# Kernel tuning notes

Measured on AMD Instinct MI355X. Metric: run time of the kernel, lower is better.

The kernel has to match this reference:

```python
import jax, jax.numpy as jnp
import numpy as np

N = 50000      # nodes
E = 800000     # edges (avg degree 16)
D_IN = 64
D_H = 64


def setup_inputs() -> dict:
    key = jax.random.key(0)
    k = jax.random.split(key, 4)
    x = jax.random.normal(k[0], (N, D_IN), dtype=jnp.float32)
    edge_index = jax.random.randint(k[1], (2, E), 0, N, dtype=jnp.int64)
    W1 = jax.random.normal(k[2], (D_IN, D_H), dtype=jnp.float32) * (1.0 / np.sqrt(D_IN))
    b1 = jnp.zeros((D_H,), dtype=jnp.float32)
    W2 = jax.random.normal(k[3], (D_H, 1), dtype=jnp.float32) * (1.0 / np.sqrt(D_H))
    b2 = jnp.zeros((1,), dtype=jnp.float32)
    return {"x": x, "edge_index": edge_index, "W1": W1, "b1": b1, "W2": W2, "b2": b2}


def gcn_conv(x, src, dst, W, b):
    """PyG-style GCNConv: linear -> symmetric-normalized scatter-aggregate + bias.
    src/dst already include self-loops."""
    n = x.shape[0]
    h = x @ W                                                   # [N, Dout]
    deg = jax.ops.segment_sum(jnp.ones_like(dst, dtype=h.dtype), dst, num_segments=n)
    dinv_sqrt = jnp.where(deg > 0, jax.lax.rsqrt(jnp.maximum(deg, 1e-12)), 0.0)
    norm = dinv_sqrt[src] * dinv_sqrt[dst]                       # [E+N]
    agg = jax.ops.segment_sum(h[src] * norm[:, None], dst, num_segments=n)
    return agg + b


def reference(x, edge_index, W1, b1, W2, b2):
    n = x.shape[0]
    loops = jnp.arange(n, dtype=edge_index.dtype)
    src = jnp.concatenate([edge_index[0], loops])                # add self-loops
    dst = jnp.concatenate([edge_index[1], loops])
    h = jax.nn.relu(gcn_conv(x, src, dst, W1, b1))               # [N, D_H]
    out = gcn_conv(h, src, dst, W2, b2)                          # [N, 1]
    return out.squeeze(-1)                                       # [N]
```

## Files before the change

kernel.cpp:

```cpp
#include <hip/hip_runtime.h>
#include <hip/hip_fp16.h>

#define D 64
#define PW2 256
#define PSH2 8
#define EPB 4096

__global__ void k_cast(const float4* __restrict__ x4, __half2* __restrict__ xh2,
                       int total4) {
    int i = blockIdx.x * blockDim.x + threadIdx.x;
    if (i < total4) {
        float4 v = x4[i];
        xh2[2 * i]     = __floats2half2_rn(v.x, v.y);
        xh2[2 * i + 1] = __floats2half2_rn(v.z, v.w);
    }
}

__global__ __launch_bounds__(256) void k_hist(const int* __restrict__ dst, int E,
                                              int* __restrict__ counts, int NP) {
    extern __shared__ int lh[];
    int t = threadIdx.x, b = blockIdx.x;
    for (int i = t; i < NP; i += 256) lh[i] = 0;
    __syncthreads();
    int base = b * EPB;
#pragma unroll
    for (int k = 0; k < EPB / 256; ++k) {
        int e = base + k * 256 + t;
        if (e < E) atomicAdd(&lh[dst[e] >> PSH2], 1);
    }
    __syncthreads();
    for (int i = t; i < NP; i += 256) counts[(size_t)b * NP + i] = lh[i];
}

__global__ __launch_bounds__(256) void k_scanA(int* __restrict__ counts, int NB, int NP,
                                               int* __restrict__ bin_total) {
    __shared__ int sh[256];
    int t = threadIdx.x, bin = blockIdx.x;
    int v = (t < NB) ? counts[(size_t)t * NP + bin] : 0;
    sh[t] = v;
    __syncthreads();
    for (int off = 1; off < 256; off <<= 1) {
        int u = (t >= off) ? sh[t - off] : 0;
        __syncthreads();
        sh[t] += u;
        __syncthreads();
    }
    if (t < NB) counts[(size_t)t * NP + bin] = sh[t] - v;
    if (t == 255) bin_total[bin] = sh[255];
}

__global__ __launch_bounds__(256) void k_scatter(const int* __restrict__ src,
        const int* __restrict__ dst, int E, const int* __restrict__ counts,
        const int* __restrict__ bin_total, int NP, int* __restrict__ csr_e) {
    __shared__ int bs[256];
    extern __shared__ int cur[];
    int t = threadIdx.x, b = blockIdx.x;
    int v = (t < NP) ? bin_total[t] : 0;
    bs[t] = v;
    __syncthreads();
    for (int off = 1; off < 256; off <<= 1) {
        int u = (t >= off) ? bs[t - off] : 0;
        __syncthreads();
        bs[t] += u;
        __syncthreads();
    }
    if (t < NP) cur[t] = counts[(size_t)b * NP + t] + (bs[t] - v);
    __syncthreads();
    int base = b * EPB;
#pragma unroll
    for (int k = 0; k < EPB / 256; ++k) {
        int e = base + k * 256 + t;
        if (e < E) {
            int s = src[e], d = dst[e];
            int pos = atomicAdd(&cur[d >> PSH2], 1);
            csr_e[pos] = s | ((d & (PW2 - 1)) << 16);
        }
    }
}

__global__ __launch_bounds__(256) void k_sort2(const int* __restrict__ csr_e,
        const int* __restrict__ bin_total, int NP, int n,
        int* __restrict__ csr_src, int* __restrict__ row_ptr,
        float* __restrict__ dinv) {
    __shared__ int bs[256];
    __shared__ int cnt[PW2];
    __shared__ int sh[PW2];
    __shared__ int cursor[PW2];
    __shared__ int s_beg, s_end;
    int t = threadIdx.x, p = blockIdx.x;
    int bv = (t < NP) ? bin_total[t] : 0;
    bs[t] = bv;
    __syncthreads();
    for (int off = 1; off < 256; off <<= 1) {
        int u = (t >= off) ? bs[t - off] : 0;
        __syncthreads();
        bs[t] += u;
        __syncthreads();
    }
    if (t == p) { s_beg = bs[t] - bv; s_end = bs[t]; }
    cnt[t] = 0;
    __syncthreads();
    int beg = s_beg, end = s_end;
    for (int i = beg + t; i < end; i += 256) atomicAdd(&cnt[csr_e[i] >> 16], 1);
    __syncthreads();
    int val = cnt[t];
    sh[t] = val;
    __syncthreads();
    for (int off = 1; off < 256; off <<= 1) {
        int u = (t >= off) ? sh[t - off] : 0;
        __syncthreads();
        sh[t] += u;
        __syncthreads();
    }
    int excl = sh[t] - val;
    cursor[t] = beg + excl;
    int node = p * PW2 + t;
    if (node <= n) {
        row_ptr[node] = beg + excl;
        if (node < n) dinv[node] = rsqrtf((float)(val + 1));
    }
    __syncthreads();
    for (int i = beg + t; i < end; i += 256) {
        int e = csr_e[i];
        int q = atomicAdd(&cursor[e >> 16], 1);
        csr_src[q] = e & 0xFFFF;
    }
}

__global__ __launch_bounds__(256) void k_gather(
        const __half2* __restrict__ xh, const float* __restrict__ x,
        const float* __restrict__ dinv, const int* __restrict__ row_ptr,
        const int* __restrict__ csr_src, float* __restrict__ agg, int n) {
    int tid = threadIdx.x;
    int wave = tid >> 6, lane = tid & 63;
    int eg = lane >> 4, dg = lane & 15;
    int v = blockIdx.x * 4 + wave;
    if (v >= n) return;
    float dv = dinv[v];
    int beg = row_ptr[v], end = row_ptr[v + 1];

    float4 acc = make_float4(0.f, 0.f, 0.f, 0.f);
    if (eg == 0) {
        float4 xv = *(const float4*)&x[(size_t)v * D + dg * 4];
        float w = dv * dv;
        acc.x = xv.x * w; acc.y = xv.y * w; acc.z = xv.z * w; acc.w = xv.w * w;
    }
    int base = beg;
    for (; base + 16 <= end; base += 16) {
        int u0 = csr_src[base + eg];
        int u1 = csr_src[base + 4 + eg];
        int u2 = csr_src[base + 8 + eg];
        int u3 = csr_src[base + 12 + eg];
        float n0 = dinv[u0] * dv, n1 = dinv[u1] * dv;
        float n2 = dinv[u2] * dv, n3 = dinv[u3] * dv;
        const __half2* p0 = xh + (size_t)u0 * 32 + dg * 2;
        const __half2* p1 = xh + (size_t)u1 * 32 + dg * 2;
        const __half2* p2 = xh + (size_t)u2 * 32 + dg * 2;
        const __half2* p3 = xh + (size_t)u3 * 32 + dg * 2;
        __half2 a0 = p0[0], b0 = p0[1];
        __half2 a1 = p1[0], b1 = p1[1];
        __half2 a2 = p2[0], b2 = p2[1];
        __half2 a3 = p3[0], b3 = p3[1];
        float2 f;
        f = __half22float2(a0); acc.x = fmaf(f.x, n0, acc.x); acc.y = fmaf(f.y, n0, acc.y);
        f = __half22float2(b0); acc.z = fmaf(f.x, n0, acc.z); acc.w = fmaf(f.y, n0, acc.w);
        f = __half22float2(a1); acc.x = fmaf(f.x, n1, acc.x); acc.y = fmaf(f.y, n1, acc.y);
        f = __half22float2(b1); acc.z = fmaf(f.x, n1, acc.z); acc.w = fmaf(f.y, n1, acc.w);
        f = __half22float2(a2); acc.x = fmaf(f.x, n2, acc.x); acc.y = fmaf(f.y, n2, acc.y);
        f = __half22float2(b2); acc.z = fmaf(f.x, n2, acc.z); acc.w = fmaf(f.y, n2, acc.w);
        f = __half22float2(a3); acc.x = fmaf(f.x, n3, acc.x); acc.y = fmaf(f.y, n3, acc.y);
        f = __half22float2(b3); acc.z = fmaf(f.x, n3, acc.z); acc.w = fmaf(f.y, n3, acc.w);
    }
    for (; base + 8 <= end; base += 8) {
        int u0 = csr_src[base + eg];
        int u1 = csr_src[base + 4 + eg];
        float n0 = dinv[u0] * dv, n1 = dinv[u1] * dv;
        const __half2* p0 = xh + (size_t)u0 * 32 + dg * 2;
        const __half2* p1 = xh + (size_t)u1 * 32 + dg * 2;
        __half2 a0 = p0[0], b0 = p0[1];
        __half2 a1 = p1[0], b1 = p1[1];
        float2 f;
        f = __half22float2(a0); acc.x = fmaf(f.x, n0, acc.x); acc.y = fmaf(f.y, n0, acc.y);
        f = __half22float2(b0); acc.z = fmaf(f.x, n0, acc.z); acc.w = fmaf(f.y, n0, acc.w);
        f = __half22float2(a1); acc.x = fmaf(f.x, n1, acc.x); acc.y = fmaf(f.y, n1, acc.y);
        f = __half22float2(b1); acc.z = fmaf(f.x, n1, acc.z); acc.w = fmaf(f.y, n1, acc.w);
    }
    for (; base < end; base += 4) {
        int idx = base + eg;
        if (idx < end) {
            int u = csr_src[idx];
            float nrm = dinv[u] * dv;
            const __half2* p0 = xh + (size_t)u * 32 + dg * 2;
            __half2 a0 = p0[0], b0 = p0[1];
            float2 f;
            f = __half22float2(a0); acc.x = fmaf(f.x, nrm, acc.x); acc.y = fmaf(f.y, nrm, acc.y);
            f = __half22float2(b0); acc.z = fmaf(f.x, nrm, acc.z); acc.w = fmaf(f.y, nrm, acc.w);
        }
    }
#pragma unroll
    for (int off = 16; off <= 32; off <<= 1) {
        acc.x += __shfl_xor(acc.x, off, 64);
        acc.y += __shfl_xor(acc.y, off, 64);
        acc.z += __shfl_xor(acc.z, off, 64);
        acc.w += __shfl_xor(acc.w, off, 64);
    }
    if (eg == 0) *(float4*)&agg[(size_t)v * D + dg * 4] = acc;
}

#define NPW 16
__global__ __launch_bounds__(256) void k_gemm(
        const float* __restrict__ agg, const float* __restrict__ dinv,
        const float* __restrict__ W1, const float* __restrict__ b1,
        const float* __restrict__ W2, float* __restrict__ sd, int n) {
    __shared__ float lrow[4][D];
    int tid = threadIdx.x;
    int wave = tid >> 6, lane = tid & 63;
    float w1c[D];
#pragma unroll
    for (int d = 0; d < D; ++d) w1c[d] = W1[d * D + lane];
    float b1l = b1[lane], w2l = W2[lane];
    int v0 = (blockIdx.x * 4 + wave) * NPW;
    for (int k = 0; k < NPW; ++k) {
        int v = v0 + k;
        if (v >= n) break;
        lrow[wave][lane] = agg[(size_t)v * D + lane];
        __builtin_amdgcn_wave_barrier();
        float h = b1l;
#pragma unroll
        for (int db = 0; db < D; db += 4) {
            float4 r = *(const float4*)&lrow[wave][db];
            h = fmaf(r.x, w1c[db], h);
            h = fmaf(r.y, w1c[db + 1], h);
            h = fmaf(r.z, w1c[db + 2], h);
            h = fmaf(r.w, w1c[db + 3], h);
        }
        float tt = fmaxf(h, 0.0f) * w2l;
#pragma unroll
        for (int off = 1; off <= 32; off <<= 1) tt += __shfl_xor(tt, off, 64);
        if (lane == 0) sd[v] = tt * dinv[v];
        __builtin_amdgcn_wave_barrier();
    }
}

__global__ __launch_bounds__(256) void k_out(const float* __restrict__ sd,
        const float* __restrict__ dinv, const int* __restrict__ row_ptr,
        const int* __restrict__ csr_src, const float* __restrict__ b2,
        float* __restrict__ out, int n) {
    int t = blockIdx.x * blockDim.x + threadIdx.x;
    int v = t >> 3, r = t & 7;
    if (v >= n) return;
    int beg = row_ptr[v], end = row_ptr[v + 1];
    float a = (r == 0) ? sd[v] : 0.0f;
    for (int i = beg + r; i < end; i += 8) a += sd[csr_src[i]];
    a += __shfl_xor(a, 1, 64);
    a += __shfl_xor(a, 2, 64);
    a += __shfl_xor(a, 4, 64);
    if (r == 0) out[v] = b2[0] + a * dinv[v];
}

extern "C" void kernel_launch(void* const* d_in, const int* in_sizes, int n_in,
                              void* d_out, int out_size, void* d_ws, size_t ws_size,
                              hipStream_t stream) {
    const float* x  = (const float*)d_in[0];
    const int*   ei = (const int*)d_in[1];
    const float* W1 = (const float*)d_in[2];
    const float* b1 = (const float*)d_in[3];
    const float* W2 = (const float*)d_in[4];
    const float* b2 = (const float*)d_in[5];

    int n = in_sizes[0] / D;
    int E = in_sizes[1] / 2;
    const int* src = ei;
    const int* dst = ei + E;

    int NP = (n + PW2 - 1) / PW2;
    int NB = (E + EPB - 1) / EPB;

    char* ws = (char*)d_ws;
    auto take = [&](size_t bytes) {
        char* p = ws;
        ws += (bytes + 255) & ~(size_t)255;
        return p;
    };
    int*     counts    = (int*)take((size_t)NB * NP * sizeof(int));
    int*     bin_total = (int*)take((size_t)NP * sizeof(int));
    int*     csr_e     = (int*)take((size_t)E * sizeof(int));
    int*     csr_src   = (int*)take((size_t)E * sizeof(int));
    int*     row_ptr   = (int*)take((size_t)(n + 1) * sizeof(int));
    float*   dinv      = (float*)take((size_t)n * sizeof(float));
    float*   sd        = (float*)take((size_t)n * sizeof(float));
    float*   agg       = (float*)take((size_t)n * D * sizeof(float));
    __half2* xh        = (__half2*)take((size_t)n * D * sizeof(__half));

    float* out = (float*)d_out;
    size_t ldsNP = (size_t)NP * sizeof(int);

    int total4 = n * D / 4;
    k_cast<<<(total4 + 255) / 256, 256, 0, stream>>>((const float4*)x, xh, total4);

    k_hist<<<NB, 256, ldsNP, stream>>>(dst, E, counts, NP);
    k_scanA<<<NP, 256, 0, stream>>>(counts, NB, NP, bin_total);
    k_scatter<<<NB, 256, ldsNP, stream>>>(src, dst, E, counts, bin_total, NP, csr_e);
    k_sort2<<<NP, 256, 0, stream>>>(csr_e, bin_total, NP, n, csr_src, row_ptr, dinv);

    k_gather<<<(n + 3) / 4, 256, 0, stream>>>(xh, x, dinv, row_ptr, csr_src, agg, n);
    k_gemm<<<(n + 4 * NPW - 1) / (4 * NPW), 256, 0, stream>>>(agg, dinv, W1, b1,
                                                              W2, sd, n);
    k_out<<<((size_t)n * 8 + 255) / 256, 256, 0, stream>>>(sd, dinv, row_ptr, csr_src,
                                                           b2, out, n);
}
```

Before: 93.60 us.

## Prescale features by dinv in cast kernel and widen gather loads to 16 bytes

```diff
diff --git a/kernel.cpp b/kernel.cpp
--- a/kernel.cpp
+++ b/kernel.cpp
@@ -6,13 +6,14 @@
 #define PSH2 8
 #define EPB 4096
 
-__global__ void k_cast(const float4* __restrict__ x4, __half2* __restrict__ xh2,
-                       int total4) {
+__global__ void k_cast(const float4* __restrict__ x4, const float* __restrict__ dinv,
+                       __half2* __restrict__ xh2, int total4) {
     int i = blockIdx.x * blockDim.x + threadIdx.x;
     if (i < total4) {
         float4 v = x4[i];
-        xh2[2 * i]     = __floats2half2_rn(v.x, v.y);
-        xh2[2 * i + 1] = __floats2half2_rn(v.z, v.w);
+        float s = dinv[i >> 4];
+        xh2[2 * i]     = __floats2half2_rn(v.x * s, v.y * s);
+        xh2[2 * i + 1] = __floats2half2_rn(v.z * s, v.w * s);
     }
 }
 
@@ -128,83 +129,63 @@
 }
 
 __global__ __launch_bounds__(256) void k_gather(
-        const __half2* __restrict__ xh, const float* __restrict__ x,
-        const float* __restrict__ dinv, const int* __restrict__ row_ptr,
-        const int* __restrict__ csr_src, float* __restrict__ agg, int n) {
+        const __half2* __restrict__ xh, const float* __restrict__ dinv,
+        const int* __restrict__ row_ptr, const int* __restrict__ csr_src,
+        float* __restrict__ agg, int n) {
     int tid = threadIdx.x;
     int wave = tid >> 6, lane = tid & 63;
-    int eg = lane >> 4, dg = lane & 15;
+    int eg = lane >> 3, dg = lane & 7;
     int v = blockIdx.x * 4 + wave;
     if (v >= n) return;
     float dv = dinv[v];
     int beg = row_ptr[v], end = row_ptr[v + 1];
 
-    float4 acc = make_float4(0.f, 0.f, 0.f, 0.f);
+    float4 A = make_float4(0.f, 0.f, 0.f, 0.f);
+    float4 B = make_float4(0.f, 0.f, 0.f, 0.f);
+    float2 f;
+#define ACC16(r)                                                        \
+    {   __half2 h0 = *(__half2*)&(r).x, h1 = *(__half2*)&(r).y,         \
+                h2 = *(__half2*)&(r).z, h3 = *(__half2*)&(r).w;         \
+        f = __half22float2(h0); A.x += f.x; A.y += f.y;                 \
+        f = __half22float2(h1); A.z += f.x; A.w += f.y;                 \
+        f = __half22float2(h2); B.x += f.x; B.y += f.y;                 \
+        f = __half22float2(h3); B.z += f.x; B.w += f.y; }
+
     if (eg == 0) {
-        float4 xv = *(const float4*)&x[(size_t)v * D + dg * 4];
-        float w = dv * dv;
-        acc.x = xv.x * w; acc.y = xv.y * w; acc.z = xv.z * w; acc.w = xv.w * w;
+        int4 r = *(const int4*)(xh + (size_t)v * 32 + dg * 4);
+        ACC16(r);
     }
     int base = beg;
     for (; base + 16 <= end; base += 16) {
         int u0 = csr_src[base + eg];
-        int u1 = csr_src[base + 4 + eg];
-        int u2 = csr_src[base + 8 + eg];
-        int u3 = csr_src[base + 12 + eg];
-        float n0 = dinv[u0] * dv, n1 = dinv[u1] * dv;
-        float n2 = dinv[u2] * dv, n3 = dinv[u3] * dv;
-        const __half2* p0 = xh + (size_t)u0 * 32 + dg * 2;
-        const __half2* p1 = xh + (size_t)u1 * 32 + dg * 2;
-        const __half2* p2 = xh + (size_t)u2 * 32 + dg * 2;
-        const __half2* p3 = xh + (size_t)u3 * 32 + dg * 2;
-        __half2 a0 = p0[0], b0 = p0[1];
-        __half2 a1 = p1[0], b1 = p1[1];
-        __half2 a2 = p2[0], b2 = p2[1];
-        __half2 a3 = p3[0], b3 = p3[1];
-        float2 f;
-        f = __half22float2(a0); acc.x = fmaf(f.x, n0, acc.x); acc.y = fmaf(f.y, n0, acc.y);
-        f = __half22float2(b0); acc.z = fmaf(f.x, n0, acc.z); acc.w = fmaf(f.y, n0, acc.w);
-        f = __half22float2(a1); acc.x = fmaf(f.x, n1, acc.x); acc.y = fmaf(f.y, n1, acc.y);
-        f = __half22float2(b1); acc.z = fmaf(f.x, n1, acc.z); acc.w = fmaf(f.y, n1, acc.w);
-        f = __half22float2(a2); acc.x = fmaf(f.x, n2, acc.x); acc.y = fmaf(f.y, n2, acc.y);
-        f = __half22float2(b2); acc.z = fmaf(f.x, n2, acc.z); acc.w = fmaf(f.y, n2, acc.w);
-        f = __half22float2(a3); acc.x = fmaf(f.x, n3, acc.x); acc.y = fmaf(f.y, n3, acc.y);
-        f = __half22float2(b3); acc.z = fmaf(f.x, n3, acc.z); acc.w = fmaf(f.y, n3, acc.w);
-    }
-    for (; base + 8 <= end; base += 8) {
-        int u0 = csr_src[base + eg];
-        int u1 = csr_src[base + 4 + eg];
-        float n0 = dinv[u0] * dv, n1 = dinv[u1] * dv;
-        const __half2* p0 = xh + (size_t)u0 * 32 + dg * 2;
-        const __half2* p1 = xh + (size_t)u1 * 32 + dg * 2;
-        __half2 a0 = p0[0], b0 = p0[1];
-        __half2 a1 = p1[0], b1 = p1[1];
-        float2 f;
-        f = __half22float2(a0); acc.x = fmaf(f.x, n0, acc.x); acc.y = fmaf(f.y, n0, acc.y);
-        f = __half22float2(b0); acc.z = fmaf(f.x, n0, acc.z); acc.w = fmaf(f.y, n0, acc.w);
-        f = __half22float2(a1); acc.x = fmaf(f.x, n1, acc.x); acc.y = fmaf(f.y, n1, acc.y);
-        f = __half22float2(b1); acc.z = fmaf(f.x, n1, acc.z); acc.w = fmaf(f.y, n1, acc.w);
-    }
-    for (; base < end; base += 4) {
+        int u1 = csr_src[base + 8 + eg];
+        int4 r0 = *(const int4*)(xh + (size_t)u0 * 32 + dg * 4);
+        int4 r1 = *(const int4*)(xh + (size_t)u1 * 32 + dg * 4);
+        ACC16(r0);
+        ACC16(r1);
+    }
+    for (; base < end; base += 8) {
         int idx = base + eg;
         if (idx < end) {
             int u = csr_src[idx];
-            float nrm = dinv[u] * dv;
-            const __half2* p0 = xh + (size_t)u * 32 + dg * 2;
-            __half2 a0 = p0[0], b0 = p0[1];
-            float2 f;
-            f = __half22float2(a0); acc.x = fmaf(f.x, nrm, acc.x); acc.y = fmaf(f.y, nrm, acc.y);
-            f = __half22float2(b0); acc.z = fmaf(f.x, nrm, acc.z); acc.w = fmaf(f.y, nrm, acc.w);
+            int4 r = *(const int4*)(xh + (size_t)u * 32 + dg * 4);
+            ACC16(r);
         }
     }
-#pragma unroll
-    for (int off = 16; off <= 32; off <<= 1) {
-        acc.x += __shfl_xor(acc.x, off, 64);
-        acc.y += __shfl_xor(acc.y, off, 64);
-        acc.z += __shfl_xor(acc.z, off, 64);
-        acc.w += __shfl_xor(acc.w, off, 64);
-    }
-    if (eg == 0) *(float4*)&agg[(size_t)v * D + dg * 4] = acc;
+#undef ACC16
+#pragma unroll
+    for (int off = 8; off <= 32; off <<= 1) {
+        A.x += __shfl_xor(A.x, off, 64); A.y += __shfl_xor(A.y, off, 64);
+        A.z += __shfl_xor(A.z, off, 64); A.w += __shfl_xor(A.w, off, 64);
+        B.x += __shfl_xor(B.x, off, 64); B.y += __shfl_xor(B.y, off, 64);
+        B.z += __shfl_xor(B.z, off, 64); B.w += __shfl_xor(B.w, off, 64);
+    }
+    if (eg == 0) {
+        A.x *= dv; A.y *= dv; A.z *= dv; A.w *= dv;
+        B.x *= dv; B.y *= dv; B.z *= dv; B.w *= dv;
+        *(float4*)&agg[(size_t)v * D + dg * 8] = A;
+        *(float4*)&agg[(size_t)v * D + dg * 8 + 4] = B;
+    }
 }
 
 #define NPW 16
@@ -295,15 +276,15 @@
     float* out = (float*)d_out;
     size_t ldsNP = (size_t)NP * sizeof(int);
 
-    int total4 = n * D / 4;
-    k_cast<<<(total4 + 255) / 256, 256, 0, stream>>>((const float4*)x, xh, total4);
-
     k_hist<<<NB, 256, ldsNP, stream>>>(dst, E, counts, NP);
     k_scanA<<<NP, 256, 0, stream>>>(counts, NB, NP, bin_total);
     k_scatter<<<NB, 256, ldsNP, stream>>>(src, dst, E, counts, bin_total, NP, csr_e);
     k_sort2<<<NP, 256, 0, stream>>>(csr_e, bin_total, NP, n, csr_src, row_ptr, dinv);
 
-    k_gather<<<(n + 3) / 4, 256, 0, stream>>>(xh, x, dinv, row_ptr, csr_src, agg, n);
+    int total4 = n * D / 4;
+    k_cast<<<(total4 + 255) / 256, 256, 0, stream>>>((const float4*)x, dinv, xh, total4);
+
+    k_gather<<<(n + 3) / 4, 256, 0, stream>>>(xh, dinv, row_ptr, csr_src, agg, n);
     k_gemm<<<(n + 4 * NPW - 1) / (4 * NPW), 256, 0, stream>>>(agg, dinv, W1, b1,
                                                               W2, sd, n);
     k_out<<<((size_t)n * 8 + 255) / 256, 256, 0, stream>>>(sd, dinv, row_ptr, csr_src,
```

New measurement: 89.17 us. -4.7%, faster.
